# Kernel tuning notes

Hardware: AMD Instinct MI355X
Metric: run time of the kernel (lower is better)

Reference implementation:

```python
import jax, jax.numpy as jnp
import numpy as np

N, U, OUT_DIM, K, B = 3960, 128, 1, 2, 16
NUM_MAT = 2 * K + 1  # 2 supports (dual random walk), K hops, + identity


def setup_inputs() -> dict:
    key = jax.random.key(0)
    ks = jax.random.split(key, 12)
    s = 0.02
    inp = {
        'inputs': jax.random.normal(ks[0], (B, N * OUT_DIM), jnp.float32),
        'adj_mx': jax.random.uniform(ks[1], (N, N), jnp.float32),
        'hidden_state': jax.random.normal(ks[2], (2, B, N * U), jnp.float32),
        'forward_index': 0,
        # layer 0: input dim = OUT_DIM (=1)
        'Wg0': s * jax.random.normal(ks[3], ((OUT_DIM + U) * NUM_MAT, 2 * U), jnp.float32),
        'bg0': jnp.ones((2 * U,), jnp.float32),  # bias_start=1.0 for gates
        'Wc0': s * jax.random.normal(ks[4], ((OUT_DIM + U) * NUM_MAT, U), jnp.float32),
        'bc0': jnp.zeros((U,), jnp.float32),
        # layer 1: input dim = U
        'Wg1': s * jax.random.normal(ks[5], ((U + U) * NUM_MAT, 2 * U), jnp.float32),
        'bg1': jnp.ones((2 * U,), jnp.float32),
        'Wc1': s * jax.random.normal(ks[6], ((U + U) * NUM_MAT, U), jnp.float32),
        'bc1': jnp.zeros((U,), jnp.float32),
        # projection Linear(rnn_units, output_dim)
        'Wp': s * jax.random.normal(ks[7], (U, OUT_DIM), jnp.float32),
        'bp': jnp.zeros((OUT_DIM,), jnp.float32),
    }
    return inp


def _random_walk(adj):
    # D^{-1} A with 0 for zero-degree rows
    d = adj.sum(axis=1)
    d_inv = jnp.where(d > 0, 1.0 / d, 0.0)
    return d_inv[:, None] * adj


def _gconv(x, h, supports, W, b):
    # x: (B,N,c_in), h: (B,N,U) -> (B,N,out)
    bsz = x.shape[0]
    cat = jnp.concatenate([x, h], axis=2)          # (B,N,C)
    C = cat.shape[2]
    x0 = cat.transpose(1, 2, 0).reshape(N, C * bsz)  # (N, C*B)
    xs = [x0]
    for S in supports:
        x1 = S @ x0
        xs.append(x1)
        xk_2, xk_1 = x0, x1
        for _ in range(2, K + 1):
            x2 = 2.0 * (S @ xk_1) - xk_2  # Chebyshev-style recurrence (as in GTS/DCRNN)
            xs.append(x2)
            xk_2, xk_1 = xk_1, x2
    xcat = jnp.stack(xs, 0)                         # (M,N,C*B)
    xcat = xcat.reshape(NUM_MAT, N, C, bsz).transpose(3, 1, 2, 0)  # (B,N,C,M)
    xcat = xcat.reshape(bsz * N, C * NUM_MAT)
    return (xcat @ W + b).reshape(bsz, N, -1)


def _dcgru_cell(x, h, supports, Wg, bg, Wc, bc):
    gates = jax.nn.sigmoid(_gconv(x, h, supports, Wg, bg))  # (B,N,2U)
    r, u = gates[..., :U], gates[..., U:]
    c = jnp.tanh(_gconv(x, r * h, supports, Wc, bc))        # (B,N,U)
    return u * h + (1.0 - u) * c


def reference(inputs, adj_mx, hidden_state, forward_index,
              Wg0, bg0, Wc0, bc0, Wg1, bg1, Wc1, bc1, Wp, bp):
    bsz = inputs.shape[0]
    supports = [_random_walk(adj_mx).T, _random_walk(adj_mx.T).T]
    x = inputs.reshape(bsz, N, OUT_DIM)
    h0 = hidden_state[0].reshape(bsz, N, U)
    h1 = hidden_state[1].reshape(bsz, N, U)
    nh0 = _dcgru_cell(x, h0, supports, Wg0, bg0, Wc0, bc0)
    nh1 = _dcgru_cell(nh0, h1, supports, Wg1, bg1, Wc1, bc1)
    out = (nh1.reshape(-1, U) @ Wp + bp).reshape(bsz, N * OUT_DIM)
    return out
```

## Files before the change

kernel.cpp:

```cpp
#include <hip/hip_runtime.h>


#define NN 3960
#define NP 3968
#define BB 16
#define UU 128
#define NT 62

typedef __attribute__((ext_vector_type(8))) short v8s;
typedef __attribute__((ext_vector_type(4))) float v4f;

__device__ __forceinline__ float bf2f(short h) {
  union { unsigned int u; float f; } v;
  v.u = ((unsigned int)(unsigned short)h) << 16;
  return v.f;
}
__device__ __forceinline__ short f2bf(float f) {
  union { float f; unsigned int u; } v; v.f = f;
  unsigned int r = (v.u + 0x7FFFu + ((v.u >> 16) & 1u)) >> 16;
  return (short)r;
}
__device__ __forceinline__ void gld16(const void* g, void* l) {
  __builtin_amdgcn_global_load_lds(
      (const __attribute__((address_space(1))) void*)g,
      (__attribute__((address_space(3))) void*)l, 16, 0, 0);
}


__global__ void k_rowsum(const float* __restrict__ A, float* __restrict__ out) {
  int i = blockIdx.x;
  float s = 0.f;
  for (int j = threadIdx.x; j < NN; j += 256) s += A[i * NN + j];
  __shared__ float red[256];
  red[threadIdx.x] = s; __syncthreads();
  for (int k = 128; k > 0; k >>= 1) {
    if (threadIdx.x < k) red[threadIdx.x] += red[threadIdx.x + k];
    __syncthreads();
  }
  if (threadIdx.x == 0) out[i] = red[0];
}

__global__ void k_colpart(const float* __restrict__ A, float* __restrict__ part) {
  int j = blockIdx.x * 256 + threadIdx.x;
  if (j >= NN) return;
  int p = blockIdx.y;
  int r0 = p * 495, r1 = r0 + 495;
  float s = 0.f;
  for (int i = r0; i < r1; i++) s += A[i * NN + j];
  part[p * NP + j] = s;
}

__global__ void k_inv(const float* __restrict__ rs, const float* __restrict__ part,
                      float* __restrict__ rinv, float* __restrict__ cinv) {
  int j = blockIdx.x * 256 + threadIdx.x;
  if (j >= NP) return;
  float r = 0.f, c = 0.f;
  if (j < NN) {
    r = rs[j];
    float s = 0.f;
    for (int p = 0; p < 8; p++) s += part[p * NP + j];
    c = s;
  }
  rinv[j] = (j < NN && r > 0.f) ? 1.f / r : 0.f;
  cinv[j] = (j < NN && c > 0.f) ? 1.f / c : 0.f;
}

__global__ void k_supports(const float* __restrict__ A, const float* __restrict__ rinv,
                           const float* __restrict__ cinv,
                           short* __restrict__ S0, short* __restrict__ S1) {
  __shared__ float t[32][33];
  int i0 = blockIdx.y * 32, j0 = blockIdx.x * 32;
  int tx = threadIdx.x, ty = threadIdx.y;
  #pragma unroll
  for (int q = 0; q < 4; q++) {
    int r = i0 + ty + 8 * q, c = j0 + tx;
    float a = (r < NN && c < NN) ? A[r * NN + c] : 0.f;
    t[ty + 8 * q][tx] = a;
    S1[r * NP + c] = f2bf(a * cinv[c]);
  }
  __syncthreads();
  #pragma unroll
  for (int q = 0; q < 4; q++) {
    int I = j0 + ty + 8 * q, J = i0 + tx;
    S0[I * NP + J] = f2bf(t[tx][ty + 8 * q] * rinv[J]);
  }
}

__global__ void k_buildH(const float* __restrict__ hs,
                         short* __restrict__ H0, short* __restrict__ H1) {
  __shared__ float t[32][33];
  int n0 = blockIdx.x * 32, u0 = blockIdx.y * 32;
  int bz = blockIdx.z; int b = bz & 15; int layer = bz >> 4;
  const float* src = hs + (size_t)(layer * BB + b) * NN * UU;
  short* H = layer ? H1 : H0;
  int tx = threadIdx.x, ty = threadIdx.y;
  #pragma unroll
  for (int q = 0; q < 4; q++) {
    int n = n0 + ty + 8 * q, u = u0 + tx;
    t[ty + 8 * q][tx] = (n < NN) ? src[n * UU + u] : 0.f;
  }
  __syncthreads();
  #pragma unroll
  for (int q = 0; q < 4; q++) {
    int u = u0 + ty + 8 * q, n = n0 + tx;
    H[(b * UU + u) * NP + n] = f2bf(t[tx][ty + 8 * q]);
  }
}

__global__ void k_buildX0x(const float* __restrict__ inp, short* __restrict__ X) {
  int n = blockIdx.x * 128 + threadIdx.x;
  int row = blockIdx.y;
  int b = row >> 5, c = row & 31;
  float v = (c == 0 && n < NN) ? inp[b * NN + n] : 0.f;
  X[row * NP + n] = f2bf(v);
}

__global__ void k_buildWt(const float* __restrict__ W, short* __restrict__ Wt,
                          int O, int KL, int CxP, int Cx) {
  int idx = blockIdx.x * 256 + threadIdx.x;
  if (idx >= O * KL) return;
  int o = idx / KL, k = idx % KL;
  int KX = 5 * CxP;
  float v = 0.f;
  if (k < KX) {
    int m = k / CxP, c = k % CxP;
    if (c < Cx) v = W[(c * 5 + m) * O + o];
  } else {
    int kl = k - KX; int m = kl >> 7, u = kl & 127;
    v = W[((Cx + u) * 5 + m) * O + o];
  }
  Wt[o * KL + k] = f2bf(v);
}

struct Bt8Args {
  const short* A[4];
  short* Y[4];
  const short* SUB[4];
  int mr[4];
};

__launch_bounds__(512, 2)
__global__ void k_gemm_bt8(Bt8Args P, const short* __restrict__ T0,
                           const short* __restrict__ T1) {
  int z = blockIdx.z;
  int row0 = blockIdx.x * 256;
  if (row0 >= P.mr[z]) return;
  const short* Ag = P.A[z];
  short* Cg = P.Y[z];
  const short* X0 = P.SUB[z];
  const short* Bg = (z & 1) ? T1 : T0;
  __shared__ short lds[65536];
  int tid = threadIdx.x, lane = tid & 63, wv = tid >> 6;
  int wr = wv >> 2, wc = wv & 3;
  int col0 = blockIdx.y * 256;

  int srow = wv * 16 + (lane >> 2);
  int scol = ((lane & 3) * 8) ^ ((lane >> 5) << 4);
  const short* aS0 = Ag + (size_t)(row0 + srow) * NP + scol;
  const short* aS1 = Ag + (size_t)(row0 + 128 + srow) * NP + scol;
  int br0 = col0 + srow;        if (br0 > NP - 1) br0 = NP - 1;
  int br1 = col0 + 128 + srow;  if (br1 > NP - 1) br1 = NP - 1;
  const short* bS0 = Bg + (size_t)br0 * NP + scol;
  const short* bS1 = Bg + (size_t)br1 * NP + scol;
  short* ldsA = lds + wv * 1024 + lane * 8;
  short* ldsB = lds + 32768 + wv * 1024 + lane * 8;

#define STG_A(buf, h, tau) do { const short* _s = ((h) ? aS1 : aS0) + (tau) * 64; \
    gld16(_s,      ldsA + (buf) * 16384 + (h) * 8192); \
    gld16(_s + 32, ldsA + (buf) * 16384 + (h) * 8192 + 512); } while (0)
#define STG_B(buf, h, tau) do { const short* _s = ((h) ? bS1 : bS0) + (tau) * 64; \
    gld16(_s,      ldsB + (buf) * 16384 + (h) * 8192); \
    gld16(_s + 32, ldsB + (buf) * 16384 + (h) * 8192 + 512); } while (0)

  int fro = (lane & 15) * 32 + (((lane >> 4) * 8) ^ ((lane & 8) * 2));
  int aBase = wr * 8192 + fro;
  int bBase = 32768 + (wc >> 1) * 8192 + (wc & 1) * 4096 + fro;

  v4f acc[8][4];
  #pragma unroll
  for (int i = 0; i < 8; i++)
    #pragma unroll
    for (int j = 0; j < 4; j++) {
      acc[i][j][0] = 0.f; acc[i][j][1] = 0.f; acc[i][j][2] = 0.f; acc[i][j][3] = 0.f;
    }
  v8s afr[4][2], bfr[4][2];

#define RD_A(b, miB) do { _Pragma("unroll") \
  for (int m2 = 0; m2 < 4; m2++) { \
    afr[m2][0] = *(const v8s*)&lds[aBase + (b) * 16384 + ((miB) + m2) * 1024]; \
    afr[m2][1] = *(const v8s*)&lds[aBase + (b) * 16384 + ((miB) + m2) * 1024 + 512]; } } while (0)
#define RD_B(b, niB) do { _Pragma("unroll") \
  for (int n2 = 0; n2 < 2; n2++) { \
    bfr[(niB) + n2][0] = *(const v8s*)&lds[bBase + (b) * 16384 + ((niB) + n2) * 1024]; \
    bfr[(niB) + n2][1] = *(const v8s*)&lds[bBase + (b) * 16384 + ((niB) + n2) * 1024 + 512]; } } while (0)
#define MM(miB, niB) do { __builtin_amdgcn_s_setprio(1); \
  _Pragma("unroll") for (int m2 = 0; m2 < 4; m2++) \
  _Pragma("unroll") for (int n2 = 0; n2 < 2; n2++) { \
    acc[(miB) + m2][(niB) + n2] = __builtin_amdgcn_mfma_f32_16x16x32_bf16( \
        afr[m2][0], bfr[(niB) + n2][0], acc[(miB) + m2][(niB) + n2], 0, 0, 0); \
    acc[(miB) + m2][(niB) + n2] = __builtin_amdgcn_mfma_f32_16x16x32_bf16( \
        afr[m2][1], bfr[(niB) + n2][1], acc[(miB) + m2][(niB) + n2], 0, 0, 0); } \
  __builtin_amdgcn_s_setprio(0); } while (0)
#define BARS do { __builtin_amdgcn_s_barrier(); __builtin_amdgcn_sched_barrier(0); } while (0)
#define VMC(n) asm volatile("s_waitcnt vmcnt(" #n ")" ::: "memory")

  STG_A(0, 0, 0); STG_A(0, 1, 0); STG_B(0, 0, 0); STG_B(0, 1, 0);
  STG_A(1, 0, 1); STG_B(1, 0, 1); STG_B(1, 1, 1);
  VMC(6);
  BARS;

  for (int it = 0; it < NT / 2; it++) {
    int t = 2 * it;
    int st1 = t + 1;
    int st2 = t + 2 > NT - 1 ? NT - 1 : t + 2;
    int st3 = t + 3 > NT - 1 ? NT - 1 : t + 3;
    RD_A(0, 0); RD_B(0, 0); STG_A(1, 1, st1); BARS; MM(0, 0); BARS;
    RD_B(0, 2); BARS; MM(0, 2); BARS;
    RD_A(0, 4); STG_B(0, 0, st2); BARS; MM(4, 0); BARS;
    STG_B(0, 1, st2); VMC(4); BARS; MM(4, 2); BARS;
    RD_A(1, 0); RD_B(1, 0); STG_A(0, 0, st2); BARS; MM(0, 0); BARS;
    RD_B(1, 2); STG_A(0, 1, st2); BARS; MM(0, 2); BARS;
    RD_A(1, 4); STG_B(1, 0, st3); BARS; MM(4, 0); BARS;
    STG_B(1, 1, st3); STG_A(1, 0, st3); VMC(6); BARS; MM(4, 2); BARS;
  }

  int cheb = X0 != nullptr;
  #pragma unroll
  for (int mi = 0; mi < 8; mi++)
    #pragma unroll
    for (int ni = 0; ni < 4; ni++) {
      int col = col0 + wc * 64 + ni * 16 + (lane & 15);
      if (col < NP) {
        #pragma unroll
        for (int r = 0; r < 4; r++) {
          int row = row0 + wr * 128 + mi * 16 + (lane >> 4) * 4 + r;
          float v = acc[mi][ni][r];
          if (cheb) v = 2.f * v - bf2f(X0[(size_t)row * NP + col]);
          Cg[(size_t)row * NP + col] = f2bf(v);
        }
      }
    }
#undef STG_A
#undef STG_B
#undef RD_A
#undef RD_B
#undef MM
#undef BARS
#undef VMC
}

__launch_bounds__(256, 2)
__global__ void k_gemm_wt(const short* __restrict__ Wt, int KL, int KX, int CxP,
                          const short* __restrict__ pX0, const short* __restrict__ pX1,
                          const short* __restrict__ pX2, const short* __restrict__ pX3,
                          const short* __restrict__ pX4,
                          const short* __restrict__ pH0, const short* __restrict__ pH1,
                          const short* __restrict__ pH2, const short* __restrict__ pH3,
                          const short* __restrict__ pH4,
                          const float* __restrict__ bias, const short* __restrict__ H,
                          short* __restrict__ Ut, short* __restrict__ out0, int epi) {
  __shared__ short lA[128 * 32];
  __shared__ short lB[128 * 40];
  int tid = threadIdx.x, lane = tid & 63, w = tid >> 6;
  int n0 = blockIdx.x * 128;
  int oy = blockIdx.y;
  int b = blockIdx.z;
  int arow = w * 16 + (lane >> 2), koff = (lane & 3) * 8;
  const short* wa0 = Wt + (oy * 128 + arow) * KL + koff;
  const short* wa1 = Wt + (oy * 128 + 64 + arow) * KL + koff;
  short* la0 = lA + w * 512 + lane * 8;
  short* la1 = lA + 2048 + w * 512 + lane * 8;
  int srow = tid >> 3, c16 = (tid & 7) * 16;
  int wr = (w >> 1) * 64, wc = (w & 1) * 64;
  v4f acc[4][4];
  #pragma unroll
  for (int i = 0; i < 4; i++)
    #pragma unroll
    for (int j = 0; j < 4; j++) {
      acc[i][j][0] = 0.f; acc[i][j][1] = 0.f; acc[i][j][2] = 0.f; acc[i][j][3] = 0.f;
    }
  int KT = KL >> 5;
  for (int kt = 0; kt < KT; kt++) {
    int kb = kt * 32;
    const short* src;
    if (kb < KX) {
      int m = kb / CxP, c0 = kb % CxP;
      const short* base = m == 0 ? pX0 : m == 1 ? pX1 : m == 2 ? pX2 : m == 3 ? pX3 : pX4;
      src = base + (b * CxP + c0) * NP;
    } else {
      int kl = kb - KX; int m = kl >> 7, c0 = kl & 127;
      const short* base = m == 0 ? pH0 : m == 1 ? pH1 : m == 2 ? pH2 : m == 3 ? pH3 : pH4;
      src = base + (b * UU + c0) * NP;
    }
    __syncthreads();
    gld16(wa0 + kb, la0); gld16(wa1 + kb, la1);
    const v8s* p = (const v8s*)(src + srow * NP + n0 + c16);
    v8s v0 = p[0], v1 = p[1];
    #pragma unroll
    for (int j = 0; j < 8; j++) {
      lB[(c16 + j) * 40 + srow] = v0[j];
      lB[(c16 + 8 + j) * 40 + srow] = v1[j];
    }
    __syncthreads();
    v8s af[4], bfv[4];
    #pragma unroll
    for (int mi = 0; mi < 4; mi++)
      af[mi] = *(const v8s*)&lA[(wr + mi * 16 + (lane & 15)) * 32 + (lane >> 4) * 8];
    #pragma unroll
    for (int ni = 0; ni < 4; ni++)
      bfv[ni] = *(const v8s*)&lB[(wc + ni * 16 + (lane & 15)) * 40 + (lane >> 4) * 8];
    #pragma unroll
    for (int mi = 0; mi < 4; mi++)
      #pragma unroll
      for (int ni = 0; ni < 4; ni++)
        acc[mi][ni] = __builtin_amdgcn_mfma_f32_16x16x32_bf16(af[mi], bfv[ni], acc[mi][ni], 0, 0, 0);
  }
  #pragma unroll
  for (int mi = 0; mi < 4; mi++)
    #pragma unroll
    for (int ni = 0; ni < 4; ni++) {
      int col = n0 + wc + ni * 16 + (lane & 15);
      #pragma unroll
      for (int r = 0; r < 4; r++) {
        int o = oy * 128 + wr + mi * 16 + (lane >> 4) * 4 + r;
        float v = acc[mi][ni][r] + bias[o];
        if (epi == 0) {
          float s = 1.f / (1.f + __expf(-v));
          if (o < UU) {
            int idx = (b * UU + o) * NP + col;
            out0[idx] = f2bf(s * bf2f(H[idx]));
          } else {
            int idx = (b * UU + (o - UU)) * NP + col;
            Ut[idx] = f2bf(s);
          }
        } else {
          float cv = tanhf(v);
          int idx = (b * UU + o) * NP + col;
          float u = bf2f(Ut[idx]), h = bf2f(H[idx]);
          out0[idx] = f2bf(u * h + (1.f - u) * cv);
        }
      }
    }
}

__global__ void k_proj(const short* __restrict__ nh, const float* __restrict__ Wp,
                       const float* __restrict__ bp, float* __restrict__ out) {
  int n = blockIdx.x * 256 + threadIdx.x;
  int b = blockIdx.y;
  if (n >= NN) return;
  float acc = bp[0];
  #pragma unroll 8
  for (int u = 0; u < UU; u++)
    acc += bf2f(nh[(b * UU + u) * NP + n]) * Wp[u];
  out[b * NN + n] = acc;
}

__global__ void k_bail(float* out, int n, float val) {
  int i = blockIdx.x * 256 + threadIdx.x;
  if (i < n) out[i] = val;
}


extern "C" void kernel_launch(void* const* d_in, const int* in_sizes, int n_in,
                              void* d_out, int out_size, void* d_ws, size_t ws_size,
                              hipStream_t stream) {
  const float* inp = (const float*)d_in[0];
  const float* adj = (const float*)d_in[1];
  const float* hid = (const float*)d_in[2];
  const float* Wg0 = (const float*)d_in[4];
  const float* bg0 = (const float*)d_in[5];
  const float* Wc0 = (const float*)d_in[6];
  const float* bc0 = (const float*)d_in[7];
  const float* Wg1 = (const float*)d_in[8];
  const float* bg1 = (const float*)d_in[9];
  const float* Wc1 = (const float*)d_in[10];
  const float* bc1 = (const float*)d_in[11];
  const float* Wp = (const float*)d_in[12];
  const float* bp = (const float*)d_in[13];
  float* out = (float*)d_out;

  const size_t SZ_S = (size_t)NP * NP * 2;
  const size_t SZ_M = (size_t)2048 * NP * 2;
  const size_t SZ_MS = (size_t)512 * NP * 2;

  size_t o_S0 = 0;
  size_t o_S1 = o_S0 + SZ_S;
  size_t o_H0 = o_S1 + SZ_S;
  size_t o_H1 = o_H0 + SZ_M;
  size_t o_Ut = o_H1 + SZ_M;
  size_t o_Xrh = o_Ut + SZ_M;
  size_t o_nh0 = o_Xrh + SZ_M;
  size_t o_YB = o_nh0 + SZ_M;
  size_t o_YX123 = o_YB + 4 * SZ_M;
  size_t o_X0x = o_YX123;
  size_t o_YS = o_X0x + SZ_MS;
  size_t o_Wg0t = o_YX123 + 3 * SZ_M;
  size_t o_Wc0t = o_Wg0t + (size_t)256 * 800 * 2;
  size_t o_Wg1t = o_Wc0t + (size_t)128 * 800 * 2;
  size_t o_Wc1t = o_Wg1t + (size_t)256 * 1280 * 2;
  size_t o_rinv = o_Wc1t + (size_t)128 * 1280 * 2;
  size_t o_cinv = o_rinv + NP * 4;
  size_t o_rs = o_cinv + NP * 4;
  size_t o_part = o_rs + NP * 4;
  size_t NEED = o_part + (size_t)8 * NP * 4;

  if (ws_size < NEED) {
    float v = -(float)(double)(ws_size >> 20);
    k_bail<<<(out_size + 255) / 256, 256, 0, stream>>>(out, out_size, v);
    return;
  }

  char* w = (char*)d_ws;
  short* S0 = (short*)(w + o_S0);
  short* S1 = (short*)(w + o_S1);
  short* H0 = (short*)(w + o_H0);
  short* H1 = (short*)(w + o_H1);
  short* Ut = (short*)(w + o_Ut);
  short* Xrh = (short*)(w + o_Xrh);
  short* nh0 = (short*)(w + o_nh0);
  short* nh1 = Ut;
  short* YB[4];
  for (int i = 0; i < 4; i++) YB[i] = (short*)(w + o_YB + i * SZ_M);
  short* YXa = H0;
  short* YXb = (short*)(w + o_YX123 + 0 * SZ_M);
  short* YXc = (short*)(w + o_YX123 + 1 * SZ_M);
  short* YXd = (short*)(w + o_YX123 + 2 * SZ_M);
  short* YS[4];
  for (int i = 0; i < 4; i++) YS[i] = (short*)(w + o_YS + i * SZ_MS);
  short* X0x = (short*)(w + o_X0x);
  short* Wg0t = (short*)(w + o_Wg0t);
  short* Wc0t = (short*)(w + o_Wc0t);
  short* Wg1t = (short*)(w + o_Wg1t);
  short* Wc1t = (short*)(w + o_Wc1t);
  float* rinv = (float*)(w + o_rinv);
  float* cinv = (float*)(w + o_cinv);
  float* rs = (float*)(w + o_rs);
  float* part = (float*)(w + o_part);

  k_rowsum<<<NN, 256, 0, stream>>>(adj, rs);
  k_colpart<<<dim3(16, 8), 256, 0, stream>>>(adj, part);
  k_inv<<<16, 256, 0, stream>>>(rs, part, rinv, cinv);
  k_supports<<<dim3(124, 124), dim3(32, 8), 0, stream>>>(adj, rinv, cinv, S0, S1);
  k_buildH<<<dim3(124, 4, 32), dim3(32, 8), 0, stream>>>(hid, H0, H1);
  k_buildX0x<<<dim3(31, 512), 128, 0, stream>>>(inp, X0x);
  k_buildWt<<<(256 * 800 + 255) / 256, 256, 0, stream>>>(Wg0, Wg0t, 256, 800, 32, 1);
  k_buildWt<<<(128 * 800 + 255) / 256, 256, 0, stream>>>(Wc0, Wc0t, 128, 800, 32, 1);
  k_buildWt<<<(256 * 1280 + 255) / 256, 256, 0, stream>>>(Wg1, Wg1t, 256, 1280, 128, 128);
  k_buildWt<<<(128 * 1280 + 255) / 256, 256, 0, stream>>>(Wc1, Wc1t, 128, 1280, 128, 128);

  auto launch_bt8 = [&](const Bt8Args& a, int nz) {
    k_gemm_bt8<<<dim3(8, 16, nz), 512, 0, stream>>>(a, S0, S1);
  };

  {
    Bt8Args h1 = {{X0x, X0x, H0, H0}, {YS[0], YS[2], YB[0], YB[2]},
                  {nullptr, nullptr, nullptr, nullptr}, {512, 512, 2048, 2048}};
    launch_bt8(h1, 4);
    Bt8Args h2 = {{YS[0], YS[2], YB[0], YB[2]}, {YS[1], YS[3], YB[1], YB[3]},
                  {X0x, X0x, H0, H0}, {512, 512, 2048, 2048}};
    launch_bt8(h2, 4);
  }
  k_gemm_wt<<<dim3(31, 2, 16), 256, 0, stream>>>(Wg0t, 800, 160, 32,
      X0x, YS[0], YS[1], YS[2], YS[3], H0, YB[0], YB[1], YB[2], YB[3],
      bg0, H0, Ut, Xrh, 0);
  {
    Bt8Args h1 = {{Xrh, Xrh, nullptr, nullptr}, {YB[0], YB[2], nullptr, nullptr},
                  {nullptr, nullptr, nullptr, nullptr}, {2048, 2048, 0, 0}};
    launch_bt8(h1, 2);
    Bt8Args h2 = {{YB[0], YB[2], nullptr, nullptr}, {YB[1], YB[3], nullptr, nullptr},
                  {Xrh, Xrh, nullptr, nullptr}, {2048, 2048, 0, 0}};
    launch_bt8(h2, 2);
  }
  k_gemm_wt<<<dim3(31, 1, 16), 256, 0, stream>>>(Wc0t, 800, 160, 32,
      X0x, YS[0], YS[1], YS[2], YS[3], Xrh, YB[0], YB[1], YB[2], YB[3],
      bc0, H0, Ut, nh0, 1);

  {
    Bt8Args h1 = {{nh0, nh0, H1, H1}, {YXa, YXc, YB[0], YB[2]},
                  {nullptr, nullptr, nullptr, nullptr}, {2048, 2048, 2048, 2048}};
    launch_bt8(h1, 4);
    Bt8Args h2 = {{YXa, YXc, YB[0], YB[2]}, {YXb, YXd, YB[1], YB[3]},
                  {nh0, nh0, H1, H1}, {2048, 2048, 2048, 2048}};
    launch_bt8(h2, 4);
  }
  k_gemm_wt<<<dim3(31, 2, 16), 256, 0, stream>>>(Wg1t, 1280, 640, 128,
      nh0, YXa, YXb, YXc, YXd, H1, YB[0], YB[1], YB[2], YB[3],
      bg1, H1, Ut, Xrh, 0);
  {
    Bt8Args h1 = {{Xrh, Xrh, nullptr, nullptr}, {YB[0], YB[2], nullptr, nullptr},
                  {nullptr, nullptr, nullptr, nullptr}, {2048, 2048, 0, 0}};
    launch_bt8(h1, 2);
    Bt8Args h2 = {{YB[0], YB[2], nullptr, nullptr}, {YB[1], YB[3], nullptr, nullptr},
                  {Xrh, Xrh, nullptr, nullptr}, {2048, 2048, 0, 0}};
    launch_bt8(h2, 2);
  }
  k_gemm_wt<<<dim3(31, 1, 16), 256, 0, stream>>>(Wc1t, 1280, 640, 128,
      nh0, YXa, YXb, YXc, YXd, Xrh, YB[0], YB[1], YB[2], YB[3],
      bc1, H1, Ut, nh1, 1);

  k_proj<<<dim3(16, 16), 256, 0, stream>>>(nh1, Wp, bp, out);
}
```

Before: 1.864 ms.

## Compact layer-0 input buffer, swizzle GEMM block order, and deconflict LDS stores

The layer-0 input matrix is shrunk from 512 padded rows (32 channels per batch) to 16 real rows plus zero padding. The input-side support GEMMs therefore process 256 rows instead of 512, and the weight GEMM reads overlapping row windows through a new batch stride, relying on zero weights for the extra channels. The support GEMM now remaps its block index so that neighbouring blocks share column tiles, aiming for better L2 reuse. The weight GEMM's transposed B tile in LDS gets an XOR swizzle to reduce bank conflicts on both the scattered stores and the vector reads. This adds index arithmetic, and the overlapping-window trick depends on every row read being finite.

Result: faster. 1.732 ms, median of 3 (-7.1%).

```diff
diff --git a/kernel.cpp b/kernel.cpp
--- a/kernel.cpp
+++ b/kernel.cpp
@@ -107,11 +107,10 @@
   }
 }
 
-__global__ void k_buildX0x(const float* __restrict__ inp, short* __restrict__ X) {
+__global__ void k_buildX0c(const float* __restrict__ inp, short* __restrict__ X) {
   int n = blockIdx.x * 128 + threadIdx.x;
   int row = blockIdx.y;
-  int b = row >> 5, c = row & 31;
-  float v = (c == 0 && n < NN) ? inp[b * NN + n] : 0.f;
+  float v = (row < BB && n < NN) ? inp[row * NN + n] : 0.f;
   X[row * NP + n] = f2bf(v);
 }
 
@@ -143,7 +142,10 @@
 __global__ void k_gemm_bt8(Bt8Args P, const short* __restrict__ T0,
                            const short* __restrict__ T1) {
   int z = blockIdx.z;
-  int row0 = blockIdx.x * 256;
+  int l = blockIdx.x + (blockIdx.y << 3);
+  int bx = l >> 4;
+  int by = ((l & 7) << 1) + ((l >> 3) & 1);
+  int row0 = bx * 256;
   if (row0 >= P.mr[z]) return;
   const short* Ag = P.A[z];
   short* Cg = P.Y[z];
@@ -152,7 +154,7 @@
   __shared__ short lds[65536];
   int tid = threadIdx.x, lane = tid & 63, wv = tid >> 6;
   int wr = wv >> 2, wc = wv & 3;
-  int col0 = blockIdx.y * 256;
+  int col0 = by * 256;
 
   int srow = wv * 16 + (lane >> 2);
   int scol = ((lane & 3) * 8) ^ ((lane >> 5) << 4);
@@ -251,6 +253,7 @@
 
 __launch_bounds__(256, 2)
 __global__ void k_gemm_wt(const short* __restrict__ Wt, int KL, int KX, int CxP,
+                          int bsx,
                           const short* __restrict__ pX0, const short* __restrict__ pX1,
                           const short* __restrict__ pX2, const short* __restrict__ pX3,
                           const short* __restrict__ pX4,
@@ -271,6 +274,7 @@
   short* la0 = lA + w * 512 + lane * 8;
   short* la1 = lA + 2048 + w * 512 + lane * 8;
   int srow = tid >> 3, c16 = (tid & 7) * 16;
+  int sk7 = srow & 7, sk3 = srow >> 3;
   int wr = (w >> 1) * 64, wc = (w & 1) * 64;
   v4f acc[4][4];
   #pragma unroll
@@ -286,7 +290,7 @@
     if (kb < KX) {
       int m = kb / CxP, c0 = kb % CxP;
       const short* base = m == 0 ? pX0 : m == 1 ? pX1 : m == 2 ? pX2 : m == 3 ? pX3 : pX4;
-      src = base + (b * CxP + c0) * NP;
+      src = base + (b * bsx + c0) * NP;
     } else {
       int kl = kb - KX; int m = kl >> 7, c0 = kl & 127;
       const short* base = m == 0 ? pH0 : m == 1 ? pH1 : m == 2 ? pH2 : m == 3 ? pH3 : pH4;
@@ -298,8 +302,9 @@
     v8s v0 = p[0], v1 = p[1];
     #pragma unroll
     for (int j = 0; j < 8; j++) {
-      lB[(c16 + j) * 40 + srow] = v0[j];
-      lB[(c16 + 8 + j) * 40 + srow] = v1[j];
+      int cA = c16 + j, cB = c16 + 8 + j;
+      lB[cA * 40 + sk7 + 8 * ((sk3 ^ (cA >> 4)) & 3)] = v0[j];
+      lB[cB * 40 + sk7 + 8 * ((sk3 ^ (cB >> 4)) & 3)] = v1[j];
     }
     __syncthreads();
     v8s af[4], bfv[4];
@@ -307,8 +312,10 @@
     for (int mi = 0; mi < 4; mi++)
       af[mi] = *(const v8s*)&lA[(wr + mi * 16 + (lane & 15)) * 32 + (lane >> 4) * 8];
     #pragma unroll
-    for (int ni = 0; ni < 4; ni++)
-      bfv[ni] = *(const v8s*)&lB[(wc + ni * 16 + (lane & 15)) * 40 + (lane >> 4) * 8];
+    for (int ni = 0; ni < 4; ni++) {
+      int colb = wc + ni * 16 + (lane & 15);
+      bfv[ni] = *(const v8s*)&lB[colb * 40 + 8 * (((lane >> 4) ^ (colb >> 4)) & 3)];
+    }
     #pragma unroll
     for (int mi = 0; mi < 4; mi++)
       #pragma unroll
@@ -392,8 +399,8 @@
   size_t o_nh0 = o_Xrh + SZ_M;
   size_t o_YB = o_nh0 + SZ_M;
   size_t o_YX123 = o_YB + 4 * SZ_M;
-  size_t o_X0x = o_YX123;
-  size_t o_YS = o_X0x + SZ_MS;
+  size_t o_X0c = o_YX123;
+  size_t o_YS = o_X0c + SZ_MS;
   size_t o_Wg0t = o_YX123 + 3 * SZ_M;
   size_t o_Wc0t = o_Wg0t + (size_t)256 * 800 * 2;
   size_t o_Wg1t = o_Wc0t + (size_t)128 * 800 * 2;
@@ -427,7 +434,7 @@
   short* YXd = (short*)(w + o_YX123 + 2 * SZ_M);
   short* YS[4];
   for (int i = 0; i < 4; i++) YS[i] = (short*)(w + o_YS + i * SZ_MS);
-  short* X0x = (short*)(w + o_X0x);
+  short* X0c = (short*)(w + o_X0c);
   short* Wg0t = (short*)(w + o_Wg0t);
   short* Wc0t = (short*)(w + o_Wc0t);
   short* Wg1t = (short*)(w + o_Wg1t);
@@ -442,7 +449,7 @@
   k_inv<<<16, 256, 0, stream>>>(rs, part, rinv, cinv);
   k_supports<<<dim3(124, 124), dim3(32, 8), 0, stream>>>(adj, rinv, cinv, S0, S1);
   k_buildH<<<dim3(124, 4, 32), dim3(32, 8), 0, stream>>>(hid, H0, H1);
-  k_buildX0x<<<dim3(31, 512), 128, 0, stream>>>(inp, X0x);
+  k_buildX0c<<<dim3(31, 256), 128, 0, stream>>>(inp, X0c);
   k_buildWt<<<(256 * 800 + 255) / 256, 256, 0, stream>>>(Wg0, Wg0t, 256, 800, 32, 1);
   k_buildWt<<<(128 * 800 + 255) / 256, 256, 0, stream>>>(Wc0, Wc0t, 128, 800, 32, 1);
   k_buildWt<<<(256 * 1280 + 255) / 256, 256, 0, stream>>>(Wg1, Wg1t, 256, 1280, 128, 128);
@@ -453,15 +460,15 @@
   };
 
   {
-    Bt8Args h1 = {{X0x, X0x, H0, H0}, {YS[0], YS[2], YB[0], YB[2]},
-                  {nullptr, nullptr, nullptr, nullptr}, {512, 512, 2048, 2048}};
+    Bt8Args h1 = {{X0c, X0c, H0, H0}, {YS[0], YS[2], YB[0], YB[2]},
+                  {nullptr, nullptr, nullptr, nullptr}, {256, 256, 2048, 2048}};
     launch_bt8(h1, 4);
     Bt8Args h2 = {{YS[0], YS[2], YB[0], YB[2]}, {YS[1], YS[3], YB[1], YB[3]},
-                  {X0x, X0x, H0, H0}, {512, 512, 2048, 2048}};
+                  {X0c, X0c, H0, H0}, {256, 256, 2048, 2048}};
     launch_bt8(h2, 4);
   }
-  k_gemm_wt<<<dim3(31, 2, 16), 256, 0, stream>>>(Wg0t, 800, 160, 32,
-      X0x, YS[0], YS[1], YS[2], YS[3], H0, YB[0], YB[1], YB[2], YB[3],
+  k_gemm_wt<<<dim3(31, 2, 16), 256, 0, stream>>>(Wg0t, 800, 160, 32, 1,
+      X0c, YS[0], YS[1], YS[2], YS[3], H0, YB[0], YB[1], YB[2], YB[3],
       bg0, H0, Ut, Xrh, 0);
   {
     Bt8Args h1 = {{Xrh, Xrh, nullptr, nullptr}, {YB[0], YB[2], nullptr, nullptr},
@@ -471,8 +478,8 @@
                   {Xrh, Xrh, nullptr, nullptr}, {2048, 2048, 0, 0}};
     launch_bt8(h2, 2);
   }
-  k_gemm_wt<<<dim3(31, 1, 16), 256, 0, stream>>>(Wc0t, 800, 160, 32,
-      X0x, YS[0], YS[1], YS[2], YS[3], Xrh, YB[0], YB[1], YB[2], YB[3],
+  k_gemm_wt<<<dim3(31, 1, 16), 256, 0, stream>>>(Wc0t, 800, 160, 32, 1,
+      X0c, YS[0], YS[1], YS[2], YS[3], Xrh, YB[0], YB[1], YB[2], YB[3],
       bc0, H0, Ut, nh0, 1);
 
   {
@@ -483,7 +490,7 @@
                   {nh0, nh0, H1, H1}, {2048, 2048, 2048, 2048}};
     launch_bt8(h2, 4);
   }
-  k_gemm_wt<<<dim3(31, 2, 16), 256, 0, stream>>>(Wg1t, 1280, 640, 128,
+  k_gemm_wt<<<dim3(31, 2, 16), 256, 0, stream>>>(Wg1t, 1280, 640, 128, 128,
       nh0, YXa, YXb, YXc, YXd, H1, YB[0], YB[1], YB[2], YB[3],
       bg1, H1, Ut, Xrh, 0);
   {
@@ -494,7 +501,7 @@
                   {Xrh, Xrh, nullptr, nullptr}, {2048, 2048, 0, 0}};
     launch_bt8(h2, 2);
   }
-  k_gemm_wt<<<dim3(31, 1, 16), 256, 0, stream>>>(Wc1t, 1280, 640, 128,
+  k_gemm_wt<<<dim3(31, 1, 16), 256, 0, stream>>>(Wc1t, 1280, 640, 128, 128,
       nh0, YXa, YXb, YXc, YXd, Xrh, YB[0], YB[1], YB[2], YB[3],
       bc1, H1, Ut, nh1, 1);
 
```
